# Optimization experiments

Measured on AMD Instinct MI355X. Metric: run time of the kernel, lower is better.

The kernel has to match this reference:

```python
import jax, jax.numpy as jnp
import numpy as np

N_OPT, OUT_F, IN_F = 16, 1024, 1024
B, A = 8, 512


def setup_inputs() -> dict:
    key = jax.random.key(0)
    k1, k2, k3, k4 = jax.random.split(key, 4)
    x = jax.random.normal(k1, (B, A, IN_F), dtype=jnp.float32)
    sp = jax.random.uniform(k2, (B, N_OPT), dtype=jnp.float32)
    selection_probs = sp / jnp.sum(sp, axis=-1, keepdims=True)
    # kaiming-uniform-ish init scale
    bound_w = 1.0 / np.sqrt(IN_F)
    weight = jax.random.uniform(k3, (N_OPT, OUT_F, IN_F), dtype=jnp.float32,
                                minval=-bound_w, maxval=bound_w)
    bias = jax.random.uniform(k4, (N_OPT, OUT_F), dtype=jnp.float32,
                              minval=-bound_w, maxval=bound_w)
    return {"x": x, "selection_probs": selection_probs, "weight": weight, "bias": bias}


def reference(x, selection_probs, weight, bias):
    # Math identical to torch forward:
    #   transformed = einsum('nij,baj->bani', weight, x)
    #   out = einsum('bani,bn->bai', transformed, selection_probs)
    # reassociated efficiently: mix weights per-example first, then one batched matmul.
    w_mixed = jnp.einsum('nij,bn->bij', weight, selection_probs)   # [B, out, in]
    out = jnp.einsum('bij,baj->bai', w_mixed, x)                   # [B, A, out]
    b_mixed = jnp.einsum('ni,bn->bi', bias, selection_probs)       # [B, out]
    return out + b_mixed[:, None, :]
```

## Files before the change

### kernel.cpp

```cpp
#include <hip/hip_runtime.h>
#include <hip/hip_bf16.h>


#define B_SZ 8
#define A_SZ 512
#define IN_F 1024
#define OUT_F 1024
#define N_OPT 16

typedef short short8 __attribute__((ext_vector_type(8)));
typedef float floatx4 __attribute__((ext_vector_type(4)));

__device__ __forceinline__ unsigned short f2bf(float f) {
    unsigned int u = __builtin_bit_cast(unsigned int, f);
    u += 0x7fffu + ((u >> 16) & 1u);
    return (unsigned short)(u >> 16);
}

#define GLOBAL_LOAD_LDS16(g, l)                                                    \
    __builtin_amdgcn_global_load_lds(                                              \
        (const __attribute__((address_space(1))) void*)(g),                        \
        (__attribute__((address_space(3))) void*)(l), 16, 0, 0)

__global__ __launch_bounds__(256) void selin_prep(
    const float* __restrict__ x, const float* __restrict__ sp,
    const float* __restrict__ weight, const float* __restrict__ bias,
    unsigned short* __restrict__ wm, unsigned short* __restrict__ xbf,
    float* __restrict__ bmixed)
{
    const int bid = blockIdx.x;
    const int tid = threadIdx.x;

    if (bid < 1024) {
        __shared__ float sps[B_SZ * N_OPT];
        if (tid < B_SZ * N_OPT) sps[tid] = sp[tid];
        __syncthreads();
        const int e4 = bid * 256 + tid;
        const float4* w4 = (const float4*)weight;
        float4 w[N_OPT];
#pragma unroll
        for (int n = 0; n < N_OPT; n++)
            w[n] = w4[(size_t)n * (IN_F * OUT_F / 4) + e4];
#pragma unroll
        for (int b = 0; b < B_SZ; b++) {
            float ax = 0.f, ay = 0.f, az = 0.f, aw = 0.f;
#pragma unroll
            for (int n = 0; n < N_OPT; n++) {
                float s = sps[b * N_OPT + n];
                ax += s * w[n].x; ay += s * w[n].y;
                az += s * w[n].z; aw += s * w[n].w;
            }
            ushort4 o = make_ushort4(f2bf(ax), f2bf(ay), f2bf(az), f2bf(aw));
            ((ushort4*)wm)[(size_t)b * (IN_F * OUT_F / 4) + e4] = o;
        }
    } else if (bid < 5120) {
        const int idx = (bid - 1024) * 256 + tid;
        float4 v = ((const float4*)x)[idx];
        ((ushort4*)xbf)[idx] = make_ushort4(f2bf(v.x), f2bf(v.y), f2bf(v.z), f2bf(v.w));
    } else {
        __shared__ float sps[B_SZ * N_OPT];
        if (tid < B_SZ * N_OPT) sps[tid] = sp[tid];
        __syncthreads();
        const int idx = (bid - 5120) * 256 + tid;
        const int b = idx >> 8, i4 = idx & 255;
        const float4* bias4 = (const float4*)bias;
        float ax = 0.f, ay = 0.f, az = 0.f, aw = 0.f;
#pragma unroll
        for (int n = 0; n < N_OPT; n++) {
            float s = sps[b * N_OPT + n];
            float4 v = bias4[n * 256 + i4];
            ax += s * v.x; ay += s * v.y; az += s * v.z; aw += s * v.w;
        }
        ((float4*)bmixed)[idx] = make_float4(ax, ay, az, aw);
    }
}

__global__ __launch_bounds__(256) void selin_gemm(
    const unsigned short* __restrict__ xbf, const unsigned short* __restrict__ wm,
    const float* __restrict__ bmixed, float* __restrict__ out)
{
    __shared__ __align__(16) unsigned short As[64 * 32];
    __shared__ __align__(16) unsigned short Bs[64 * 32];

    const int tid = threadIdx.x;
    const int bid = blockIdx.x;
    const int b   = bid & 7;
    const int t   = bid >> 3;
    const int mb  = t & 7;
    const int nb  = t >> 3;
    const int m0  = mb * 64, n0 = nb * 64;

    const unsigned short* Ag = xbf + ((size_t)b * A_SZ  + m0) * IN_F;
    const unsigned short* Bg = wm  + ((size_t)b * OUT_F + n0) * IN_F;

    const int ga = (tid >> 2) * IN_F + (tid & 3) * 8;

    const int lane = tid & 63;
    const int wv   = tid >> 6;
    const int wmi  = wv >> 1, wni = wv & 1;
    const int lm   = lane & 15, kq = lane >> 4;

    floatx4 acc[2][2];
#pragma unroll
    for (int i = 0; i < 2; i++)
#pragma unroll
        for (int j = 0; j < 2; j++)
            acc[i][j] = (floatx4){0.f, 0.f, 0.f, 0.f};

    for (int k0 = 0; k0 < IN_F; k0 += 32) {
        GLOBAL_LOAD_LDS16(Ag + ga + k0, &As[tid * 8]);
        GLOBAL_LOAD_LDS16(Bg + ga + k0, &Bs[tid * 8]);
        __syncthreads();

        short8 a[2], bb[2];
#pragma unroll
        for (int mi = 0; mi < 2; mi++)
            a[mi] = *(const short8*)&As[(wmi * 32 + mi * 16 + lm) * 32 + kq * 8];
#pragma unroll
        for (int ni = 0; ni < 2; ni++)
            bb[ni] = *(const short8*)&Bs[(wni * 32 + ni * 16 + lm) * 32 + kq * 8];

#pragma unroll
        for (int mi = 0; mi < 2; mi++)
#pragma unroll
            for (int ni = 0; ni < 2; ni++)
                acc[mi][ni] = __builtin_amdgcn_mfma_f32_16x16x32_bf16(
                    a[mi], bb[ni], acc[mi][ni], 0, 0, 0);
        __syncthreads();
    }

#pragma unroll
    for (int ni = 0; ni < 2; ni++) {
        const int gcol = n0 + wni * 32 + ni * 16 + lm;
        const float bv = bmixed[b * OUT_F + gcol];
#pragma unroll
        for (int mi = 0; mi < 2; mi++) {
            const int grow = m0 + wmi * 32 + mi * 16 + kq * 4;
            float* op = out + ((size_t)b * A_SZ + grow) * OUT_F + gcol;
#pragma unroll
            for (int r = 0; r < 4; r++)
                op[(size_t)r * OUT_F] = acc[mi][ni][r] + bv;
        }
    }
}

extern "C" void kernel_launch(void* const* d_in, const int* in_sizes, int n_in,
                              void* d_out, int out_size, void* d_ws, size_t ws_size,
                              hipStream_t stream) {
    const float* x      = (const float*)d_in[0];
    const float* sp     = (const float*)d_in[1];
    const float* weight = (const float*)d_in[2];
    const float* bias   = (const float*)d_in[3];
    float* out = (float*)d_out;

    unsigned short* wm  = (unsigned short*)d_ws;
    unsigned short* xbf = wm + (size_t)B_SZ * OUT_F * IN_F;
    float* bmixed       = (float*)(xbf + (size_t)B_SZ * A_SZ * IN_F);

    selin_prep<<<5128, 256, 0, stream>>>(x, sp, weight, bias, wm, xbf, bmixed);
    selin_gemm<<<1024, 256, 0, stream>>>(xbf, wm, bmixed, out);
}
```

Before: 131.6 us.

## Pre-swizzle operands into MFMA fragment layout and drop LDS staging in GEMM

The prep kernel now writes the mixed weights and bf16 activations in a K-chunked layout where each 8-element k-group per row is contiguous. The GEMM can then load MFMA fragments straight from global memory without LDS or barriers. The GEMM moves from 16x16x32 to 32x32x16 MFMA with a 32x256 block tile, each wave covering 32x64, and the grid halves to 512 blocks. Operand reuse now comes only from caches, and each wave issues strided global loads with no shared-memory reuse across waves.

```diff
diff --git a/kernel.cpp b/kernel.cpp
--- a/kernel.cpp
+++ b/kernel.cpp
@@ -9,7 +9,7 @@
 #define N_OPT 16
 
 typedef short short8 __attribute__((ext_vector_type(8)));
-typedef float floatx4 __attribute__((ext_vector_type(4)));
+typedef float floatx16 __attribute__((ext_vector_type(16)));
 
 __device__ __forceinline__ unsigned short f2bf(float f) {
     unsigned int u = __builtin_bit_cast(unsigned int, f);
@@ -17,15 +17,10 @@
     return (unsigned short)(u >> 16);
 }
 
-#define GLOBAL_LOAD_LDS16(g, l)                                                    \
-    __builtin_amdgcn_global_load_lds(                                              \
-        (const __attribute__((address_space(1))) void*)(g),                        \
-        (__attribute__((address_space(3))) void*)(l), 16, 0, 0)
-
 __global__ __launch_bounds__(256) void selin_prep(
     const float* __restrict__ x, const float* __restrict__ sp,
     const float* __restrict__ weight, const float* __restrict__ bias,
-    unsigned short* __restrict__ wm, unsigned short* __restrict__ xbf,
+    unsigned short* __restrict__ wt, unsigned short* __restrict__ xt,
     float* __restrict__ bmixed)
 {
     const int bid = blockIdx.x;
@@ -35,12 +30,18 @@
         __shared__ float sps[B_SZ * N_OPT];
         if (tid < B_SZ * N_OPT) sps[tid] = sp[tid];
         __syncthreads();
-        const int e4 = bid * 256 + tid;
+        const int ib = bid & 127, kb = bid >> 7;
+        const int i0 = ib * 8, q0 = kb * 32;
+        const int i_loc = tid & 7;
+        const int q_loc = tid >> 3;
         const float4* w4 = (const float4*)weight;
         float4 w[N_OPT];
 #pragma unroll
         for (int n = 0; n < N_OPT; n++)
-            w[n] = w4[(size_t)n * (IN_F * OUT_F / 4) + e4];
+            w[n] = w4[(size_t)n * (IN_F * OUT_F / 4) + (i0 + i_loc) * (IN_F / 4) + q0 + q_loc];
+        const int c_glob = kb * 16 + (q_loc >> 1);
+        ushort4* wt4 = (ushort4*)wt;
+        const size_t widx = ((size_t)c_glob * OUT_F + i0 + i_loc) * 2 + (q_loc & 1);
 #pragma unroll
         for (int b = 0; b < B_SZ; b++) {
             float ax = 0.f, ay = 0.f, az = 0.f, aw = 0.f;
@@ -50,18 +51,32 @@
                 ax += s * w[n].x; ay += s * w[n].y;
                 az += s * w[n].z; aw += s * w[n].w;
             }
-            ushort4 o = make_ushort4(f2bf(ax), f2bf(ay), f2bf(az), f2bf(aw));
-            ((ushort4*)wm)[(size_t)b * (IN_F * OUT_F / 4) + e4] = o;
+            wt4[(size_t)b * (OUT_F * IN_F / 4) + widx] =
+                make_ushort4(f2bf(ax), f2bf(ay), f2bf(az), f2bf(aw));
         }
-    } else if (bid < 5120) {
-        const int idx = (bid - 1024) * 256 + tid;
-        float4 v = ((const float4*)x)[idx];
-        ((ushort4*)xbf)[idx] = make_ushort4(f2bf(v.x), f2bf(v.y), f2bf(v.z), f2bf(v.w));
+    } else if (bid < 3072) {
+        const int t2 = bid - 1024;
+        const int b  = t2 >> 8;
+        const int rem = t2 & 255;
+        const int r0 = (rem & 31) * 16;
+        const int c0 = (rem >> 5) * 16;
+        const int w  = tid >> 6, l = tid & 63;
+        const int r  = r0 + w * 4 + (l >> 4);
+        const int c  = c0 + (l & 15);
+        const float4* x4 = (const float4*)x;
+        const size_t rbase = ((size_t)b * A_SZ + r) * (IN_F / 4) + c * 2;
+        float4 v0 = x4[rbase], v1 = x4[rbase + 1];
+        short8 o;
+        o[0] = (short)f2bf(v0.x); o[1] = (short)f2bf(v0.y);
+        o[2] = (short)f2bf(v0.z); o[3] = (short)f2bf(v0.w);
+        o[4] = (short)f2bf(v1.x); o[5] = (short)f2bf(v1.y);
+        o[6] = (short)f2bf(v1.z); o[7] = (short)f2bf(v1.w);
+        *(short8*)(xt + ((size_t)b * 65536 + (size_t)c * A_SZ + r) * 8) = o;
     } else {
         __shared__ float sps[B_SZ * N_OPT];
         if (tid < B_SZ * N_OPT) sps[tid] = sp[tid];
         __syncthreads();
-        const int idx = (bid - 5120) * 256 + tid;
+        const int idx = (bid - 3072) * 256 + tid;
         const int b = idx >> 8, i4 = idx & 255;
         const float4* bias4 = (const float4*)bias;
         float ax = 0.f, ay = 0.f, az = 0.f, aw = 0.f;
@@ -76,71 +91,51 @@
 }
 
 __global__ __launch_bounds__(256) void selin_gemm(
-    const unsigned short* __restrict__ xbf, const unsigned short* __restrict__ wm,
+    const unsigned short* __restrict__ xt, const unsigned short* __restrict__ wt,
     const float* __restrict__ bmixed, float* __restrict__ out)
 {
-    __shared__ __align__(16) unsigned short As[64 * 32];
-    __shared__ __align__(16) unsigned short Bs[64 * 32];
+    const int tid  = threadIdx.x;
+    const int bid  = blockIdx.x;
+    const int b    = bid & 7;
+    const int t    = bid >> 3;
+    const int ms   = t & 15;
+    const int ns   = t >> 4;
+    const int wv   = tid >> 6;
+    const int lane = tid & 63;
+    const int lm   = lane & 31;
+    const int kq   = lane >> 5;
 
-    const int tid = threadIdx.x;
-    const int bid = blockIdx.x;
-    const int b   = bid & 7;
-    const int t   = bid >> 3;
-    const int mb  = t & 7;
-    const int nb  = t >> 3;
-    const int m0  = mb * 64, n0 = nb * 64;
+    const int r0 = ms * 32;
+    const int n0 = ns * 256 + wv * 64;
 
-    const unsigned short* Ag = xbf + ((size_t)b * A_SZ  + m0) * IN_F;
-    const unsigned short* Bg = wm  + ((size_t)b * OUT_F + n0) * IN_F;
+    const unsigned short* xtb = xt + (size_t)b * 524288;
+    const unsigned short* wtb = wt + (size_t)b * 1048576;
 
-    const int ga = (tid >> 2) * IN_F + (tid & 3) * 8;
+    const unsigned short* ap = xtb + (size_t)kq * 4096 + (size_t)(r0 + lm) * 8;
+    const unsigned short* bp = wtb + (size_t)kq * 8192 + (size_t)(n0 + lm) * 8;
 
-    const int lane = tid & 63;
-    const int wv   = tid >> 6;
-    const int wmi  = wv >> 1, wni = wv & 1;
-    const int lm   = lane & 15, kq = lane >> 4;
+    floatx16 acc0 = {0.f}, acc1 = {0.f};
+#pragma unroll
+    for (int i = 0; i < 16; i++) { acc0[i] = 0.f; acc1[i] = 0.f; }
 
-    floatx4 acc[2][2];
-#pragma unroll
-    for (int i = 0; i < 2; i++)
-#pragma unroll
-        for (int j = 0; j < 2; j++)
-            acc[i][j] = (floatx4){0.f, 0.f, 0.f, 0.f};
-
-    for (int k0 = 0; k0 < IN_F; k0 += 32) {
-        GLOBAL_LOAD_LDS16(Ag + ga + k0, &As[tid * 8]);
-        GLOBAL_LOAD_LDS16(Bg + ga + k0, &Bs[tid * 8]);
-        __syncthreads();
-
-        short8 a[2], bb[2];
-#pragma unroll
-        for (int mi = 0; mi < 2; mi++)
-            a[mi] = *(const short8*)&As[(wmi * 32 + mi * 16 + lm) * 32 + kq * 8];
-#pragma unroll
-        for (int ni = 0; ni < 2; ni++)
-            bb[ni] = *(const short8*)&Bs[(wni * 32 + ni * 16 + lm) * 32 + kq * 8];
-
-#pragma unroll
-        for (int mi = 0; mi < 2; mi++)
-#pragma unroll
-            for (int ni = 0; ni < 2; ni++)
-                acc[mi][ni] = __builtin_amdgcn_mfma_f32_16x16x32_bf16(
-                    a[mi], bb[ni], acc[mi][ni], 0, 0, 0);
-        __syncthreads();
+#pragma unroll 4
+    for (int s = 0; s < 64; s++) {
+        short8 a  = *(const short8*)(ap + (size_t)s * 8192);
+        short8 b0 = *(const short8*)(bp + (size_t)s * 16384);
+        short8 b1 = *(const short8*)(bp + (size_t)s * 16384 + 256);
+        acc0 = __builtin_amdgcn_mfma_f32_32x32x16_bf16(a, b0, acc0, 0, 0, 0);
+        acc1 = __builtin_amdgcn_mfma_f32_32x32x16_bf16(a, b1, acc1, 0, 0, 0);
     }
 
+    const int gcol0 = n0 + lm;
+    const float bv0 = bmixed[b * OUT_F + gcol0];
+    const float bv1 = bmixed[b * OUT_F + gcol0 + 32];
 #pragma unroll
-    for (int ni = 0; ni < 2; ni++) {
-        const int gcol = n0 + wni * 32 + ni * 16 + lm;
-        const float bv = bmixed[b * OUT_F + gcol];
-#pragma unroll
-        for (int mi = 0; mi < 2; mi++) {
-            const int grow = m0 + wmi * 32 + mi * 16 + kq * 4;
-            float* op = out + ((size_t)b * A_SZ + grow) * OUT_F + gcol;
-#pragma unroll
-            for (int r = 0; r < 4; r++)
-                op[(size_t)r * OUT_F] = acc[mi][ni][r] + bv;
-        }
+    for (int reg = 0; reg < 16; reg++) {
+        const int grow = r0 + (reg & 3) + 8 * (reg >> 2) + 4 * kq;
+        float* op = out + ((size_t)b * A_SZ + grow) * OUT_F + gcol0;
+        op[0]  = acc0[reg] + bv0;
+        op[32] = acc1[reg] + bv1;
     }
 }
 
@@ -153,10 +148,10 @@
     const float* bias   = (const float*)d_in[3];
     float* out = (float*)d_out;
 
-    unsigned short* wm  = (unsigned short*)d_ws;
-    unsigned short* xbf = wm + (size_t)B_SZ * OUT_F * IN_F;
-    float* bmixed       = (float*)(xbf + (size_t)B_SZ * A_SZ * IN_F);
+    unsigned short* wt  = (unsigned short*)d_ws;
+    unsigned short* xt  = wt + (size_t)B_SZ * OUT_F * IN_F;
+    float* bmixed       = (float*)(xt + (size_t)B_SZ * A_SZ * IN_F);
 
-    selin_prep<<<5128, 256, 0, stream>>>(x, sp, weight, bias, wm, xbf, bmixed);
-    selin_gemm<<<1024, 256, 0, stream>>>(xbf, wm, bmixed, out);
+    selin_prep<<<3080, 256, 0, stream>>>(x, sp, weight, bias, wt, xt, bmixed);
+    selin_gemm<<<512, 256, 0, stream>>>(xt, wt, bmixed, out);
 }
```

Measured after the change: 137.6 us. 4.5% more time.
